# Kernel optimization log

Measured on AMD Instinct MI355X. Metric: run time of the kernel, lower is better.

The kernel has to match this reference:

```python
import math
import jax, jax.numpy as jnp
import numpy as np

N_TOKENS = 2048
HIDDEN = 2880
HEAD_DIM = 64
N_HEADS = 64
N_KV = 8
Q_MULT = N_HEADS // N_KV  # 8
SLIDING_WINDOW = 128      # layer_idx=0 -> even -> window active
RMS_EPS = 1e-5
SM_SCALE = 1.0 / math.sqrt(HEAD_DIM)
ROPE_THETA = 150000.0
INIT_CTX = 4096
SCALING_FACTOR = 32.0
NTK_ALPHA = 1.0
NTK_BETA = 32.0
QKV_DIM = HEAD_DIM * (N_HEADS + 2 * N_KV)  # 5120


def _rope_cos_sin(n_tokens):
    # YaRN/NTK-scaled inverse frequencies (scaling_factor > 1 branch)
    freq = ROPE_THETA ** (jnp.arange(0, HEAD_DIM, 2, dtype=jnp.float32) / HEAD_DIM)
    concentration = 0.1 * math.log(SCALING_FACTOR) + 1.0
    d_half = HEAD_DIM / 2
    low = d_half * math.log(INIT_CTX / (NTK_BETA * 2 * math.pi)) / math.log(ROPE_THETA)
    high = d_half * math.log(INIT_CTX / (NTK_ALPHA * 2 * math.pi)) / math.log(ROPE_THETA)
    interpolation = 1.0 / (SCALING_FACTOR * freq)
    extrapolation = 1.0 / freq
    ramp = (jnp.arange(d_half, dtype=jnp.float32) - low) / (high - low)
    mask = 1.0 - jnp.clip(ramp, 0.0, 1.0)
    inv_freq = interpolation * (1.0 - mask) + extrapolation * mask
    pos = jnp.arange(n_tokens, dtype=jnp.float32)
    freqs = pos[:, None] * inv_freq[None, :]        # [n, d/2]
    return jnp.cos(freqs) * concentration, jnp.sin(freqs) * concentration


def _apply_rotary(x, cos, sin):
    # x: [n, h, d]; cos/sin: [n, d/2]
    c = cos[:, None, :]
    s = sin[:, None, :]
    x1, x2 = jnp.split(x, 2, axis=-1)
    return jnp.concatenate([x1 * c - x2 * s, x2 * c + x1 * s], axis=-1)


def setup_inputs() -> dict:
    key = jax.random.key(0)
    ks = jax.random.split(key, 4)
    x = jax.random.normal(ks[0], (N_TOKENS, HIDDEN), dtype=jnp.float32)
    norm_scale = jnp.ones((HIDDEN,), dtype=jnp.float32)
    sinks = jax.random.normal(ks[1], (N_HEADS,), dtype=jnp.float32)
    w_qkv = jax.random.normal(ks[2], (QKV_DIM, HIDDEN), dtype=jnp.float32) * 0.02
    b_qkv = jnp.zeros((QKV_DIM,), dtype=jnp.float32)
    w_out = jax.random.normal(ks[3], (HIDDEN, N_HEADS * HEAD_DIM), dtype=jnp.float32) * 0.02
    b_out = jnp.zeros((HIDDEN,), dtype=jnp.float32)
    return {"x": x, "norm_scale": norm_scale, "sinks": sinks,
            "w_qkv": w_qkv, "b_qkv": b_qkv, "w_out": w_out, "b_out": b_out}


def reference(x, norm_scale, sinks, w_qkv, b_qkv, w_out, b_out):
    n = x.shape[0]
    # RMSNorm (fp32 math as in original)
    t = x.astype(jnp.float32)
    t = t * jax.lax.rsqrt(jnp.mean(t * t, axis=-1, keepdims=True) + RMS_EPS)
    t = (t * norm_scale).astype(x.dtype)
    # QKV projection (torch Linear: y = x @ W^T + b)
    qkv = t @ w_qkv.T + b_qkv
    q = qkv[:, : N_HEADS * HEAD_DIM].reshape(n, N_KV, Q_MULT, HEAD_DIM)
    k = qkv[:, N_HEADS * HEAD_DIM:(N_HEADS + N_KV) * HEAD_DIM].reshape(n, N_KV, HEAD_DIM)
    v = qkv[:, (N_HEADS + N_KV) * HEAD_DIM:].reshape(n, N_KV, HEAD_DIM)
    # RoPE
    cos, sin = _rope_cos_sin(n)
    q = _apply_rotary(q.reshape(n, N_HEADS, HEAD_DIM), cos, sin).reshape(n, N_KV, Q_MULT, HEAD_DIM)
    k = _apply_rotary(k, cos, sin)
    # GQA attention scores: [kv_heads, q_mult, q, k]
    qk = jnp.einsum('qhmd,khd->hmqk', q, k) * SM_SCALE
    # causal + sliding-window mask: allow j <= i and j > i - SLIDING_WINDOW
    i = jnp.arange(n)[:, None]
    j = jnp.arange(n)[None, :]
    allowed = (j <= i) & (j > i - SLIDING_WINDOW)
    neg_inf = jnp.asarray(-jnp.inf, dtype=qk.dtype)
    qk = jnp.where(allowed[None, None, :, :], qk, neg_inf)
    # append learned sink logit per head, softmax, then drop sink column
    sink_logits = jnp.broadcast_to(
        sinks.reshape(N_KV, Q_MULT, 1, 1), (N_KV, Q_MULT, n, 1)).astype(qk.dtype)
    logits = jnp.concatenate([qk, sink_logits], axis=-1)
    weights = jax.nn.softmax(logits, axis=-1)[..., :-1]
    attn = jnp.einsum('hmqk,khd->qhmd', weights, v).reshape(n, N_HEADS * HEAD_DIM)
    return x + attn @ w_out.T + b_out
```

## Files before the change

### kernel.cpp

```cpp
#include <hip/hip_runtime.h>
#include <hip/hip_bf16.h>
#include <math.h>

typedef __attribute__((ext_vector_type(8))) short short8;
typedef __attribute__((ext_vector_type(4))) float f32x4;

#define NTOK 2048
#define HID  2880
#define QKVD 5120
#define KOFF 4096
#define VOFF 4608
#define ATTD 4096

__device__ __forceinline__ unsigned short f2bf(float f) {
  union { float f; unsigned int u; } v; v.f = f;
  unsigned int u = v.u;
  unsigned int r = (u + 0x7FFFu + ((u >> 16) & 1u)) >> 16;
  return (unsigned short)r;
}
__device__ __forceinline__ float bf2f(unsigned short h) {
  union { unsigned int u; float f; } v; v.u = ((unsigned int)h) << 16; return v.f;
}
__device__ __forceinline__ void gload_lds16(const unsigned short* g, unsigned short* l) {
  __builtin_amdgcn_global_load_lds(
      (const __attribute__((address_space(1))) unsigned int*)g,
      (__attribute__((address_space(3))) unsigned int*)l, 16, 0, 0);
}
#define MFMA16(a, b, c) __builtin_amdgcn_mfma_f32_16x16x32_bf16((a), (b), (c), 0, 0, 0)

__global__ void rope_table_kernel(float* __restrict__ ctab, float* __restrict__ stab) {
  int idx = blockIdx.x * 256 + threadIdx.x;
  if (idx >= NTOK * 32) return;
  int pos = idx >> 5, i = idx & 31;
  const double theta = 150000.0;
  const double two_pi = 6.283185307179586476925286766559;
  double freq = pow(theta, (double)i / 32.0);
  double interp = 1.0 / (32.0 * freq);
  double extrap = 1.0 / freq;
  double low  = 32.0 * log(4096.0 / (32.0 * two_pi)) / log(theta);
  double high = 32.0 * log(4096.0 / (1.0  * two_pi)) / log(theta);
  double ramp = ((double)i - low) / (high - low);
  ramp = ramp < 0.0 ? 0.0 : (ramp > 1.0 ? 1.0 : ramp);
  double maskv = 1.0 - ramp;
  double inv = interp * (1.0 - maskv) + extrap * maskv;
  double ang = (double)pos * inv;
  double conc = 0.1 * log(32.0) + 1.0;
  ctab[idx] = (float)(cos(ang) * conc);
  stab[idx] = (float)(sin(ang) * conc);
}

__global__ __launch_bounds__(256) void rmsnorm_kernel(
    const float* __restrict__ x, const float* __restrict__ scale,
    unsigned short* __restrict__ t) {
  int row = blockIdx.x;
  const float4* xr = (const float4*)(x + (size_t)row * HID);
  const float4* sc = (const float4*)scale;
  float ss = 0.f;
  for (int c = threadIdx.x; c < HID / 4; c += 256) {
    float4 v = xr[c];
    ss += v.x * v.x + v.y * v.y + v.z * v.z + v.w * v.w;
  }
  #pragma unroll
  for (int m = 1; m < 64; m <<= 1) ss += __shfl_xor(ss, m);
  __shared__ float red[4];
  if ((threadIdx.x & 63) == 0) red[threadIdx.x >> 6] = ss;
  __syncthreads();
  float tot = red[0] + red[1] + red[2] + red[3];
  float rs = rsqrtf(tot / (float)HID + 1e-5f);
  for (int c = threadIdx.x; c < HID / 4; c += 256) {
    float4 v = xr[c];
    float4 s4 = sc[c];
    ushort4 o;
    o.x = f2bf(v.x * rs * s4.x); o.y = f2bf(v.y * rs * s4.y);
    o.z = f2bf(v.z * rs * s4.z); o.w = f2bf(v.w * rs * s4.w);
    *(ushort4*)&t[(size_t)row * HID + c * 4] = o;
  }
}

__global__ __launch_bounds__(256) void cvt_w_kernel(
    const float* __restrict__ w, unsigned short* __restrict__ wb, long total4) {
  long idx = (long)blockIdx.x * 256 + threadIdx.x;
  if (idx >= total4) return;
  long base = idx * 4;
  float4 v = *(const float4*)&w[base];
  ushort4 o;
  o.x = f2bf(v.x); o.y = f2bf(v.y); o.z = f2bf(v.z); o.w = f2bf(v.w);
  *(ushort4*)&wb[base] = o;
}

template<int BN, bool RESID>
__global__ __launch_bounds__(256, 2) void gemm_kernel(
    const unsigned short* __restrict__ A, const unsigned short* __restrict__ B,
    const float* __restrict__ bias, const float* __restrict__ resid,
    void* __restrict__ Cout, int K, int NC) {
  constexpr int NF = BN / 32;
  __shared__ unsigned short sA[2][8192];
  __shared__ unsigned short sB[2][BN * 64];

  const int tid = threadIdx.x;
  const int q8 = gridDim.x >> 3;
  const int sw = ((int)blockIdx.x & 7) * q8 + ((int)blockIdx.x >> 3);
  const int m0 = (sw & 15) * 128;
  const int n0 = (sw >> 4) * BN;

  const int lane = tid & 63, wid = tid >> 6;
  const int fr = lane & 15, fq = lane >> 4;
  const int wr = wid >> 1, wc = wid & 1;
  const int swz = (fr & 7) << 4;
  const int r_st = tid >> 3;
  const int c8_st = ((tid & 7) ^ ((tid >> 3) & 7)) * 8;
  const int wlds = wid << 9;

  const unsigned short* Ag = A + (size_t)(m0 + r_st) * K + c8_st;
  const unsigned short* Bg = B + (size_t)(n0 + r_st) * K + c8_st;

  f32x4 acc[4][NF] = {};
  const int NT = K >> 6;

  auto LDA_ = [&](int bs, int mf, int ks) -> short8 {
    int row = wr * 64 + mf * 16 + fr;
    int cb = (ks * 64 + fq * 16) ^ swz;
    return *(const short8*)((const char*)&sA[bs][0] + row * 128 + cb);
  };
  auto LDB_ = [&](int bs, int nf, int ks) -> short8 {
    int row = wc * (NF * 16) + nf * 16 + fr;
    int cb = (ks * 64 + fq * 16) ^ swz;
    return *(const short8*)((const char*)&sB[bs][0] + row * 128 + cb);
  };
  auto issue_tile = [&](int tt, int b) {
    const unsigned short* Agt = Ag + (size_t)tt * 64;
    const unsigned short* Bgt = Bg + (size_t)tt * 64;
    #pragma unroll
    for (int s = 0; s < 4; ++s)
      gload_lds16(Agt + (size_t)(s * 32) * K, &sA[b][s * 2048 + wlds]);
    #pragma unroll
    for (int s = 0; s < NF; ++s)
      gload_lds16(Bgt + (size_t)(s * 32) * K, &sB[b][s * 2048 + wlds]);
  };

  issue_tile(0, 0);

  for (int t = 0; t < NT; ++t) {
    const int cu = t & 1;
    if (t + 1 < NT) {
      issue_tile(t + 1, cu ^ 1);
      if constexpr (NF == 5) asm volatile("s_waitcnt vmcnt(9)" ::: "memory");
      else                   asm volatile("s_waitcnt vmcnt(7)" ::: "memory");
    } else {
      asm volatile("s_waitcnt vmcnt(0)" ::: "memory");
    }
    __builtin_amdgcn_s_barrier();
    __builtin_amdgcn_sched_barrier(0);
    short8 afr0[4], bfr0[NF], afr1[4], bfr1[NF];
    #pragma unroll
    for (int mf = 0; mf < 4; ++mf) afr0[mf] = LDA_(cu, mf, 0);
    #pragma unroll
    for (int nf = 0; nf < NF; ++nf) bfr0[nf] = LDB_(cu, nf, 0);
    #pragma unroll
    for (int mf = 0; mf < 4; ++mf) afr1[mf] = LDA_(cu, mf, 1);
    #pragma unroll
    for (int nf = 0; nf < NF; ++nf) bfr1[nf] = LDB_(cu, nf, 1);
    __builtin_amdgcn_s_setprio(1);
    #pragma unroll
    for (int mf = 0; mf < 4; ++mf)
      #pragma unroll
      for (int nf = 0; nf < NF; ++nf)
        acc[mf][nf] = MFMA16(afr0[mf], bfr0[nf], acc[mf][nf]);
    #pragma unroll
    for (int mf = 0; mf < 4; ++mf)
      #pragma unroll
      for (int nf = 0; nf < NF; ++nf)
        acc[mf][nf] = MFMA16(afr1[mf], bfr1[nf], acc[mf][nf]);
    __builtin_amdgcn_s_setprio(0);
    __builtin_amdgcn_s_barrier();
  }

  if (!RESID) {
    unsigned short* C = (unsigned short*)Cout;
    #pragma unroll
    for (int mf = 0; mf < 4; ++mf)
      #pragma unroll
      for (int nf = 0; nf < NF; ++nf)
        #pragma unroll
        for (int r = 0; r < 4; ++r) {
          int row = m0 + wr * 64 + mf * 16 + fq * 4 + r;
          int col = n0 + wc * (NF * 16) + nf * 16 + fr;
          C[(size_t)row * NC + col] = f2bf(acc[mf][nf][r] + bias[col]);
        }
  } else {
    float* C = (float*)Cout;
    #pragma unroll
    for (int mf = 0; mf < 4; ++mf)
      #pragma unroll
      for (int nf = 0; nf < NF; ++nf)
        #pragma unroll
        for (int r = 0; r < 4; ++r) {
          int row = m0 + wr * 64 + mf * 16 + fq * 4 + r;
          int col = n0 + wc * (NF * 16) + nf * 16 + fr;
          C[(size_t)row * NC + col] = acc[mf][nf][r] + bias[col] + resid[(size_t)row * NC + col];
        }
  }
}

__global__ __launch_bounds__(256) void attn_kernel(
    const unsigned short* __restrict__ qkv, const float* __restrict__ sinks,
    const float* __restrict__ ctab, const float* __restrict__ stab,
    unsigned short* __restrict__ attn) {
  const int tile = blockIdx.x;
  const int gh = blockIdx.y;
  const int h = gh >> 3;
  const int q0 = tile * 64;
  const int kbase = q0 - 127;

  __shared__ unsigned short Qsh[64][72];
  __shared__ unsigned short Ksh[192][72];
  __shared__ unsigned short Vt[64][200];
  __shared__ float rowpart[4][64];
  __shared__ float invsum[64];
  unsigned short (*Wsh)[200] = (unsigned short (*)[200])Ksh;

  const int tid = threadIdx.x;

  {
    int r = tid >> 2, cp = tid & 3;
    int i = q0 + r;
    const unsigned short* qp = &qkv[(size_t)i * QKVD + gh * 64 + cp * 8];
    short8 xa = *(const short8*)qp;
    short8 xb = *(const short8*)(qp + 32);
    short8 oa, ob;
    #pragma unroll
    for (int e = 0; e < 8; ++e) {
      float c = ctab[i * 32 + cp * 8 + e], s = stab[i * 32 + cp * 8 + e];
      float x1 = bf2f((unsigned short)xa[e]), x2 = bf2f((unsigned short)xb[e]);
      oa[e] = (short)f2bf(x1 * c - x2 * s);
      ob[e] = (short)f2bf(x2 * c + x1 * s);
    }
    *(short8*)&Qsh[r][cp * 8] = oa;
    *(short8*)&Qsh[r][cp * 8 + 32] = ob;
  }
  #pragma unroll
  for (int it = 0; it < 3; ++it) {
    int lin = tid + it * 256;
    int r = lin >> 2, cp = lin & 3;
    int j = kbase + r;
    short8 oa = {}, ob = {};
    if (j >= 0 && j < NTOK) {
      const unsigned short* kp = &qkv[(size_t)j * QKVD + KOFF + h * 64 + cp * 8];
      short8 xa = *(const short8*)kp;
      short8 xb = *(const short8*)(kp + 32);
      #pragma unroll
      for (int e = 0; e < 8; ++e) {
        float c = ctab[j * 32 + cp * 8 + e], s = stab[j * 32 + cp * 8 + e];
        float x1 = bf2f((unsigned short)xa[e]), x2 = bf2f((unsigned short)xb[e]);
        oa[e] = (short)f2bf(x1 * c - x2 * s);
        ob[e] = (short)f2bf(x2 * c + x1 * s);
      }
    }
    *(short8*)&Ksh[r][cp * 8] = oa;
    *(short8*)&Ksh[r][cp * 8 + 32] = ob;
  }
  #pragma unroll
  for (int c = 0; c < 6; ++c) {
    int lin = tid + c * 256;
    int r = lin >> 3, ch = (lin & 7) * 8;
    int j = kbase + r;
    uint4 v = make_uint4(0u, 0u, 0u, 0u);
    if (j >= 0 && j < NTOK) v = *(const uint4*)&qkv[(size_t)j * QKVD + VOFF + h * 64 + ch];
    const unsigned short* vs = (const unsigned short*)&v;
    #pragma unroll
    for (int i2 = 0; i2 < 8; ++i2) Vt[ch + i2][r] = vs[i2];
  }
  __syncthreads();

  const int lane = tid & 63;
  const int wid = tid >> 6;
  const int fr = lane & 15;
  const int fq = lane >> 4;
  const int fc = fq * 8;
  const int wk0 = wid * 48;

  f32x4 sc[4][3] = {};
  #pragma unroll
  for (int k0 = 0; k0 < 64; k0 += 32) {
    short8 qa[4], kb[3];
    #pragma unroll
    for (int mi = 0; mi < 4; ++mi) qa[mi] = *(const short8*)&Qsh[mi * 16 + fr][k0 + fc];
    #pragma unroll
    for (int ni = 0; ni < 3; ++ni) kb[ni] = *(const short8*)&Ksh[wk0 + ni * 16 + fr][k0 + fc];
    #pragma unroll
    for (int mi = 0; mi < 4; ++mi)
      #pragma unroll
      for (int ni = 0; ni < 3; ++ni)
        sc[mi][ni] = MFMA16(qa[mi], kb[ni], sc[mi][ni]);
  }

  float rsum[4][4];
  #pragma unroll
  for (int mi = 0; mi < 4; ++mi)
    #pragma unroll
    for (int r = 0; r < 4; ++r) {
      int i = q0 + mi * 16 + fq * 4 + r;
      float rs = 0.f;
      #pragma unroll
      for (int ni = 0; ni < 3; ++ni) {
        int kk = wk0 + ni * 16 + fr;
        int j = kbase + kk;
        bool valid = (j >= 0) && (j <= i) && (j > i - 128);
        float pw = valid ? __expf(sc[mi][ni][r] * 0.125f) : 0.f;
        sc[mi][ni][r] = pw;
        rs += pw;
      }
      rs += __shfl_xor(rs, 1);
      rs += __shfl_xor(rs, 2);
      rs += __shfl_xor(rs, 4);
      rs += __shfl_xor(rs, 8);
      rsum[mi][r] = rs;
    }

  __syncthreads();

  #pragma unroll
  for (int mi = 0; mi < 4; ++mi)
    #pragma unroll
    for (int r = 0; r < 4; ++r) {
      int row = mi * 16 + fq * 4 + r;
      #pragma unroll
      for (int ni = 0; ni < 3; ++ni)
        Wsh[row][wk0 + ni * 16 + fr] = f2bf(sc[mi][ni][r]);
      if (fr == 0) rowpart[wid][row] = rsum[mi][r];
    }
  __syncthreads();

  if (tid < 64) {
    float tot = rowpart[0][tid] + rowpart[1][tid] + rowpart[2][tid] + rowpart[3][tid];
    invsum[tid] = 1.f / (tot + __expf(sinks[gh]));
  }

  f32x4 pv[4] = {};
  #pragma unroll
  for (int k0 = 0; k0 < 192; k0 += 32) {
    short8 pa[4];
    #pragma unroll
    for (int mi = 0; mi < 4; ++mi) pa[mi] = *(const short8*)&Wsh[mi * 16 + fr][k0 + fc];
    short8 vb = *(const short8*)&Vt[wid * 16 + fr][k0 + fc];
    #pragma unroll
    for (int mi = 0; mi < 4; ++mi)
      pv[mi] = MFMA16(pa[mi], vb, pv[mi]);
  }
  __syncthreads();

  #pragma unroll
  for (int mi = 0; mi < 4; ++mi)
    #pragma unroll
    for (int r = 0; r < 4; ++r) {
      int row = mi * 16 + fq * 4 + r;
      float inv = invsum[row];
      int col = wid * 16 + fr;
      attn[(size_t)(q0 + row) * ATTD + gh * 64 + col] = f2bf(pv[mi][r] * inv);
    }
}

extern "C" void kernel_launch(void* const* d_in, const int* in_sizes, int n_in,
                              void* d_out, int out_size, void* d_ws, size_t ws_size,
                              hipStream_t stream) {
  const float* x          = (const float*)d_in[0];
  const float* norm_scale = (const float*)d_in[1];
  const float* sinks      = (const float*)d_in[2];
  const float* w_qkv      = (const float*)d_in[3];
  const float* b_qkv      = (const float*)d_in[4];
  const float* w_out      = (const float*)d_in[5];
  const float* b_out      = (const float*)d_in[6];
  float* out = (float*)d_out;

  char* ws = (char*)d_ws;
  unsigned short* qkv_bf = (unsigned short*)(ws);
  unsigned short* t_bf   = (unsigned short*)(ws + 20971520);
  unsigned short* attn_b = (unsigned short*)(ws + 20971520);
  unsigned short* wbf    = (unsigned short*)(ws + 20971520 + 16777216);
  float*          ctab   = (float*)(ws + 20971520 + 16777216 + 29491200);
  float*          stab   = ctab + NTOK * 32;

  rope_table_kernel<<<dim3(256), dim3(256), 0, stream>>>(ctab, stab);
  rmsnorm_kernel<<<dim3(NTOK), dim3(256), 0, stream>>>(x, norm_scale, t_bf);
  cvt_w_kernel<<<dim3(14400), dim3(256), 0, stream>>>(w_qkv, wbf, 3686400L);
  gemm_kernel<160, false><<<dim3(512), dim3(256), 0, stream>>>(
      t_bf, wbf, b_qkv, nullptr, (void*)qkv_bf, HID, QKVD);
  attn_kernel<<<dim3(32, 64), dim3(256), 0, stream>>>(qkv_bf, sinks, ctab, stab, attn_b);
  cvt_w_kernel<<<dim3(11520), dim3(256), 0, stream>>>(w_out, wbf, 2949120L);
  gemm_kernel<96, true><<<dim3(480), dim3(256), 0, stream>>>(
      attn_b, wbf, b_out, x, (void*)out, ATTD, HID);
}
```

Baseline: 208.3 us.

## Merge weight conversions into one launch and restructure GEMM prefetch barrier

Both weight matrices are converted to bf16 in a single kernel launch, with separate workspace buffers, so one launch and its tail are removed. The GEMM main loop now waits for all loads and barriers once per iteration, then issues the next tile's prefetch. This drops the trailing barrier at the cost of less overlap between outstanding loads and the barrier wait. The single barrier still protects the buffer being overwritten, because the prefetch targets the buffer read in the previous iteration and is issued after all waves pass the barrier.

```diff
diff --git a/kernel.cpp b/kernel.cpp
--- a/kernel.cpp
+++ b/kernel.cpp
@@ -77,15 +77,19 @@
   }
 }
 
-__global__ __launch_bounds__(256) void cvt_w_kernel(
-    const float* __restrict__ w, unsigned short* __restrict__ wb, long total4) {
+__global__ __launch_bounds__(256) void cvt_both_kernel(
+    const float* __restrict__ w1, const float* __restrict__ w2,
+    unsigned short* __restrict__ o1, unsigned short* __restrict__ o2,
+    long n1_4, long total4) {
   long idx = (long)blockIdx.x * 256 + threadIdx.x;
   if (idx >= total4) return;
-  long base = idx * 4;
-  float4 v = *(const float4*)&w[base];
+  const float* src; unsigned short* dst; long base;
+  if (idx < n1_4) { src = w1; dst = o1; base = idx * 4; }
+  else            { src = w2; dst = o2; base = (idx - n1_4) * 4; }
+  float4 v = *(const float4*)&src[base];
   ushort4 o;
   o.x = f2bf(v.x); o.y = f2bf(v.y); o.z = f2bf(v.z); o.w = f2bf(v.w);
-  *(ushort4*)&wb[base] = o;
+  *(ushort4*)&dst[base] = o;
 }
 
 template<int BN, bool RESID>
@@ -142,15 +146,10 @@
 
   for (int t = 0; t < NT; ++t) {
     const int cu = t & 1;
-    if (t + 1 < NT) {
-      issue_tile(t + 1, cu ^ 1);
-      if constexpr (NF == 5) asm volatile("s_waitcnt vmcnt(9)" ::: "memory");
-      else                   asm volatile("s_waitcnt vmcnt(7)" ::: "memory");
-    } else {
-      asm volatile("s_waitcnt vmcnt(0)" ::: "memory");
-    }
+    asm volatile("s_waitcnt vmcnt(0)" ::: "memory");
     __builtin_amdgcn_s_barrier();
     __builtin_amdgcn_sched_barrier(0);
+    if (t + 1 < NT) issue_tile(t + 1, cu ^ 1);
     short8 afr0[4], bfr0[NF], afr1[4], bfr1[NF];
     #pragma unroll
     for (int mf = 0; mf < 4; ++mf) afr0[mf] = LDA_(cu, mf, 0);
@@ -172,7 +171,6 @@
       for (int nf = 0; nf < NF; ++nf)
         acc[mf][nf] = MFMA16(afr1[mf], bfr1[nf], acc[mf][nf]);
     __builtin_amdgcn_s_setprio(0);
-    __builtin_amdgcn_s_barrier();
   }
 
   if (!RESID) {
@@ -376,17 +374,19 @@
   unsigned short* qkv_bf = (unsigned short*)(ws);
   unsigned short* t_bf   = (unsigned short*)(ws + 20971520);
   unsigned short* attn_b = (unsigned short*)(ws + 20971520);
-  unsigned short* wbf    = (unsigned short*)(ws + 20971520 + 16777216);
-  float*          ctab   = (float*)(ws + 20971520 + 16777216 + 29491200);
-  float*          stab   = ctab + NTOK * 32;
+  unsigned short* w1bf   = (unsigned short*)(ws + 20971520 + 16777216);
+  unsigned short* w2bf   = w1bf;
+  w2bf = (unsigned short*)(ws + 20971520 + 16777216 + 29491200);
+  float* ctab = (float*)(ws + 20971520 + 16777216 + 29491200 + 23592960);
+  float* stab = ctab + NTOK * 32;
 
   rope_table_kernel<<<dim3(256), dim3(256), 0, stream>>>(ctab, stab);
   rmsnorm_kernel<<<dim3(NTOK), dim3(256), 0, stream>>>(x, norm_scale, t_bf);
-  cvt_w_kernel<<<dim3(14400), dim3(256), 0, stream>>>(w_qkv, wbf, 3686400L);
+  cvt_both_kernel<<<dim3(25920), dim3(256), 0, stream>>>(
+      w_qkv, w_out, w1bf, w2bf, 3686400L, 6635520L);
   gemm_kernel<160, false><<<dim3(512), dim3(256), 0, stream>>>(
-      t_bf, wbf, b_qkv, nullptr, (void*)qkv_bf, HID, QKVD);
+      t_bf, w1bf, b_qkv, nullptr, (void*)qkv_bf, HID, QKVD);
   attn_kernel<<<dim3(32, 64), dim3(256), 0, stream>>>(qkv_bf, sinks, ctab, stab, attn_b);
-  cvt_w_kernel<<<dim3(11520), dim3(256), 0, stream>>>(w_out, wbf, 2949120L);
   gemm_kernel<96, true><<<dim3(480), dim3(256), 0, stream>>>(
-      attn_b, wbf, b_out, x, (void*)out, ATTD, HID);
-}
+      attn_b, w2bf, b_out, x, (void*)out, ATTD, HID);
+}
```

Measured after the change: 209.0 us. No clear change (+0.3%).
